# Kernel optimization log

Hardware: AMD Instinct MI355X
Metric: run time of the kernel (lower is better)

## Reference

```python
import jax, jax.numpy as jnp
import numpy as np

MARGIN = 1.0
EPS = 1e-8  # torch F.cosine_similarity default eps


def setup_inputs() -> dict:
    key = jax.random.key(0)
    k1, k2 = jax.random.split(key)
    reps = jax.random.normal(k1, (8192, 512), dtype=jnp.float32)
    labels = jax.random.randint(k2, (8192,), 0, 100, dtype=jnp.int64)
    return {"reps": reps, "labels": labels}


def reference(reps, labels):
    # cosine_similarity(reps[None, :, :], reps[:, None, :], dim=2)
    # == dot(a,b) / (max(||a||,eps) * max(||b||,eps)); compute via normalize + GEMM
    norms = jnp.maximum(jnp.linalg.norm(reps, axis=1, keepdims=True), EPS)
    xn = reps / norms  # [N, D]
    cos_sim = xn @ xn.T  # [N, N]
    label_matrix = labels[None, :] == labels[:, None]  # [N, N] bool
    same_class_loss = jnp.where(label_matrix, (1.0 - cos_sim) ** 2, 0.0)
    diff_class_loss = jnp.where(label_matrix, 0.0,
                                jnp.maximum(MARGIN - cos_sim, 0.0) ** 2)
    loss = same_class_loss + diff_class_loss
    return loss.mean()
```

## Files before the change

kernel.cpp:

```cpp
#include <hip/hip_runtime.h>


typedef __attribute__((ext_vector_type(8))) short  s8;
typedef __attribute__((ext_vector_type(8))) __bf16 bf8;
typedef __attribute__((ext_vector_type(4))) float  f4;
typedef __attribute__((ext_vector_type(4))) unsigned short u4v;

#define NT32 136
#define KOUT 16
#define KCW  512

#define OFF_XT  0u
#define OFF_INV (8u * 1024u * 1024u)
#define OFF_S   (OFF_INV + 8192u * 4u)
#define OFF_S2  (OFF_S + 512u * 4u)
#define OFF_TK  (OFF_S2 + 4u)
#define OFF_GP  (OFF_S2 + 64u)

__device__ __forceinline__ unsigned short f2bf(float f) {
    union { float f; unsigned u; } v; v.f = f;
    unsigned r = v.u + 0x7FFFu + ((v.u >> 16) & 1u);
    return (unsigned short)(r >> 16);
}

__global__ __launch_bounds__(256) void k_norms(
    const float* __restrict__ reps, float* __restrict__ inv,
    float* __restrict__ zbuf )
{
    const int t = threadIdx.x, lane = t & 63, w = t >> 6;
    if (blockIdx.x == 0) {
        for (int z = t; z < 514; z += 256) zbuf[z] = 0.f;
    }
    const int row = blockIdx.x * 4 + w;
    const float4 x0 = *(const float4*)(reps + (size_t)row * 512 + lane * 4);
    const float4 x1 = *(const float4*)(reps + (size_t)row * 512 + 256 + lane * 4);
    float ss = x0.x*x0.x + x0.y*x0.y + x0.z*x0.z + x0.w*x0.w
             + x1.x*x1.x + x1.y*x1.y + x1.z*x1.z + x1.w*x1.w;
    #pragma unroll
    for (int off = 1; off < 64; off <<= 1) ss += __shfl_xor(ss, off, 64);
    if (lane == 0) inv[row] = 1.0f / fmaxf(sqrtf(ss), 1e-8f);
}

__global__ __launch_bounds__(256) void k_norm_transpose(
    const float* __restrict__ reps, const float* __restrict__ inv,
    unsigned short* __restrict__ xt, float* __restrict__ svec)
{
    __shared__ unsigned short tile[64][72];
    __shared__ float sred[4][64];
    const int t = threadIdx.x, lane = t & 63, w = t >> 6;
    const int a0 = blockIdx.x * 64, i0 = blockIdx.y * 64;
    const int colg = t & 15;
    const int ig0  = t >> 4;

    float4 sa = {0.f, 0.f, 0.f, 0.f};
    #pragma unroll
    for (int j = 0; j < 4; ++j) {
        const int il = ig0 + j * 16;
        const float iv = inv[i0 + il];
        const float4 x = *(const float4*)(reps + (size_t)(i0 + il) * 512 + a0 + colg * 4);
        const float4 xn = {x.x * iv, x.y * iv, x.z * iv, x.w * iv};
        sa.x += xn.x; sa.y += xn.y; sa.z += xn.z; sa.w += xn.w;
        ushort4 p;
        p.x = f2bf(xn.x); p.y = f2bf(xn.y); p.z = f2bf(xn.z); p.w = f2bf(xn.w);
        *(ushort4*)&tile[il][colg * 4] = p;
    }
    __syncthreads();

    {
        const int ig = t & 15, ag = t >> 4;
        u4v rows[4];
        #pragma unroll
        for (int r = 0; r < 4; ++r)
            rows[r] = *(const u4v*)&tile[ig * 4 + r][ag * 4];
        #pragma unroll
        for (int j = 0; j < 4; ++j) {
            ushort4 o;
            o.x = (unsigned short)rows[0][j];
            o.y = (unsigned short)rows[1][j];
            o.z = (unsigned short)rows[2][j];
            o.w = (unsigned short)rows[3][j];
            *(ushort4*)(xt + (size_t)(a0 + ag * 4 + j) * 8192 + i0 + ig * 4) = o;
        }
    }

    sa.x += __shfl_xor(sa.x, 16, 64); sa.x += __shfl_xor(sa.x, 32, 64);
    sa.y += __shfl_xor(sa.y, 16, 64); sa.y += __shfl_xor(sa.y, 32, 64);
    sa.z += __shfl_xor(sa.z, 16, 64); sa.z += __shfl_xor(sa.z, 32, 64);
    sa.w += __shfl_xor(sa.w, 16, 64); sa.w += __shfl_xor(sa.w, 32, 64);
    if (lane < 16) {
        sred[w][lane * 4 + 0] = sa.x; sred[w][lane * 4 + 1] = sa.y;
        sred[w][lane * 4 + 2] = sa.z; sred[w][lane * 4 + 3] = sa.w;
    }
    __syncthreads();
    if (t < 64) {
        const float v = sred[0][t] + sred[1][t] + sred[2][t] + sred[3][t];
        atomicAdd(&svec[a0 + t], v);
    }
}

__global__ __launch_bounds__(64) void k_gram(
    const unsigned short* __restrict__ xt, float* __restrict__ gp)
{
    const int lane = threadIdx.x;
    const int l15 = lane & 15, l4 = lane >> 4;
    int tt = blockIdx.x, ta = 0;
    while (tt >= 16 - ta) { tt -= 16 - ta; ++ta; }
    const int tb = ta + tt;
    const int k0 = blockIdx.y * KCW;
    const unsigned short* Arow = xt + (size_t)(ta * 32 + l15) * 8192;
    const unsigned short* Brow = xt + (size_t)(tb * 32 + l15) * 8192;

    f4 acc[2][2];
    #pragma unroll
    for (int mi = 0; mi < 2; ++mi)
        #pragma unroll
        for (int ni = 0; ni < 2; ++ni) {
            f4 z = {0.f, 0.f, 0.f, 0.f};
            acc[mi][ni] = z;
        }

    for (int k = 0; k < KCW; k += 32) {
        const int ko = k0 + k + l4 * 8;
        s8 af[2], bfr[2];
        af[0]  = *(const s8*)(Arow + ko);
        af[1]  = *(const s8*)(Arow + (size_t)16 * 8192 + ko);
        bfr[0] = *(const s8*)(Brow + ko);
        bfr[1] = *(const s8*)(Brow + (size_t)16 * 8192 + ko);
        #pragma unroll
        for (int mi = 0; mi < 2; ++mi)
            #pragma unroll
            for (int ni = 0; ni < 2; ++ni)
                acc[mi][ni] = __builtin_amdgcn_mfma_f32_16x16x32_bf16(
                    __builtin_bit_cast(bf8, af[mi]),
                    __builtin_bit_cast(bf8, bfr[ni]),
                    acc[mi][ni], 0, 0, 0);
    }

    float* gb = gp + ((size_t)blockIdx.y * NT32 + blockIdx.x) * 1024;
    #pragma unroll
    for (int mi = 0; mi < 2; ++mi)
        #pragma unroll
        for (int ni = 0; ni < 2; ++ni)
            #pragma unroll
            for (int r = 0; r < 4; ++r) {
                const int a_ = mi * 16 + l4 * 4 + r;
                const int b_ = ni * 16 + l15;
                gb[a_ * 32 + b_] = acc[mi][ni][r];
            }
}

__global__ __launch_bounds__(256) void k_reduce_final(
    const float* __restrict__ gp, const float* __restrict__ svec,
    float* __restrict__ s2, int* __restrict__ ticket,
    float* __restrict__ out)
{
    __shared__ float part[4];
    __shared__ int lastFlag;
    const int t = threadIdx.x;
    const int c = blockIdx.x * 256 + t;
    const f4* g4 = (const f4*)gp;
    f4 s = {0.f, 0.f, 0.f, 0.f};
    #pragma unroll
    for (int p = 0; p < KOUT; ++p) s += g4[(size_t)p * (NT32 * 256) + c];
    int tt = c >> 8, ta = 0;
    while (tt >= 16 - ta) { tt -= 16 - ta; ++ta; }
    const float wgt = (tt == 0) ? 1.f : 2.f;
    float sq = wgt * (s.x * s.x + s.y * s.y + s.z * s.z + s.w * s.w);
    #pragma unroll
    for (int off = 1; off < 64; off <<= 1) sq += __shfl_xor(sq, off, 64);
    if ((t & 63) == 0) part[t >> 6] = sq;
    __syncthreads();
    if (t == 0) {
        atomicAdd(s2, part[0] + part[1] + part[2] + part[3]);
        __threadfence();
        lastFlag = (atomicAdd(ticket, 1) == (int)gridDim.x - 1);
    }
    __syncthreads();
    if (lastFlag) {
        __threadfence();
        const float v0 = svec[t], v1 = svec[t + 256];
        float p = v0 * v0 + v1 * v1;
        #pragma unroll
        for (int off = 1; off < 64; off <<= 1) p += __shfl_xor(p, off, 64);
        if ((t & 63) == 0) part[t >> 6] = p;
        __syncthreads();
        if (t == 0) {
            const float s1 = part[0] + part[1] + part[2] + part[3];
            const float S2 = atomicAdd(s2, 0.f);
            const double NN = 67108864.0;
            out[0] = (float)((NN - 2.0 * (double)s1 + (double)S2) / NN);
        }
    }
}

extern "C" void kernel_launch(void* const* d_in, const int* in_sizes, int n_in,
                              void* d_out, int out_size, void* d_ws, size_t ws_size,
                              hipStream_t stream)
{
    const float* reps = (const float*)d_in[0];
    char* ws = (char*)d_ws;
    unsigned short* xt   = (unsigned short*)(ws + OFF_XT);
    float*          invn = (float*)(ws + OFF_INV);
    float*          svec = (float*)(ws + OFF_S);
    float*          s2   = (float*)(ws + OFF_S2);
    int*            tick = (int*)(ws + OFF_TK);
    float*          gp   = (float*)(ws + OFF_GP);

    k_norms<<<2048, 256, 0, stream>>>(reps, invn, svec);
    k_norm_transpose<<<dim3(8, 128), 256, 0, stream>>>(reps, invn, xt, svec);
    k_gram<<<dim3(NT32, KOUT), 64, 0, stream>>>(xt, gp);
    k_reduce_final<<<NT32, 256, 0, stream>>>(gp, svec, s2, tick, (float*)d_out);
}
```

Baseline: 98.70 us.

## Split Gram K-reduction finer, remap blocks per XCD, widen final reduction grid

The Gram kernel now splits the 8192-long reduction into 32 chunks instead of 16, which doubles the number of blocks. It uses a 1D grid whose block index is remapped so that all K-chunks of a tile land on the same XCD, sharing L2 for the A/B rows, and it adds an occupancy hint and unroll. The final reduction launches 1088 blocks, each summing a slice of partials across K-planes through LDS instead of 136 blocks doing 16 serial loads. The transpose's padded LDS tile is replaced by an XOR-swizzled layout. The intent is more parallelism and better cache locality, at the cost of twice the partial-sum traffic.

```diff
diff --git a/kernel.cpp b/kernel.cpp
--- a/kernel.cpp
+++ b/kernel.cpp
@@ -7,8 +7,10 @@
 typedef __attribute__((ext_vector_type(4))) unsigned short u4v;
 
 #define NT32 136
-#define KOUT 16
-#define KCW  512
+#define KOUT 32
+#define KCW  256
+#define PLANE_F4 (NT32 * 256)
+#define RB 1088
 
 #define OFF_XT  0u
 #define OFF_INV (8u * 1024u * 1024u)
@@ -45,7 +47,7 @@
     const float* __restrict__ reps, const float* __restrict__ inv,
     unsigned short* __restrict__ xt, float* __restrict__ svec)
 {
-    __shared__ unsigned short tile[64][72];
+    __shared__ unsigned short tile[64 * 64];
     __shared__ float sred[4][64];
     const int t = threadIdx.x, lane = t & 63, w = t >> 6;
     const int a0 = blockIdx.x * 64, i0 = blockIdx.y * 64;
@@ -62,7 +64,7 @@
         sa.x += xn.x; sa.y += xn.y; sa.z += xn.z; sa.w += xn.w;
         ushort4 p;
         p.x = f2bf(xn.x); p.y = f2bf(xn.y); p.z = f2bf(xn.z); p.w = f2bf(xn.w);
-        *(ushort4*)&tile[il][colg * 4] = p;
+        *(ushort4*)&tile[il * 64 + ((colg * 4) ^ (((il >> 2) & 7) << 3))] = p;
     }
     __syncthreads();
 
@@ -71,7 +73,7 @@
         u4v rows[4];
         #pragma unroll
         for (int r = 0; r < 4; ++r)
-            rows[r] = *(const u4v*)&tile[ig * 4 + r][ag * 4];
+            rows[r] = *(const u4v*)&tile[(ig * 4 + r) * 64 + ((ag * 4) ^ ((ig & 7) << 3))];
         #pragma unroll
         for (int j = 0; j < 4; ++j) {
             ushort4 o;
@@ -98,55 +100,49 @@
     }
 }
 
-__global__ __launch_bounds__(64) void k_gram(
+__global__ __launch_bounds__(64, 4) void k_gram(
     const unsigned short* __restrict__ xt, float* __restrict__ gp)
 {
     const int lane = threadIdx.x;
     const int l15 = lane & 15, l4 = lane >> 4;
-    int tt = blockIdx.x, ta = 0;
+    const int lin = blockIdx.x;
+    const int xcd = lin & 7, j = lin >> 3;
+    const int tIdx = xcd * 17 + (j >> 5);
+    const int kc   = j & 31;
+    int tt = tIdx, ta = 0;
     while (tt >= 16 - ta) { tt -= 16 - ta; ++ta; }
     const int tb = ta + tt;
-    const int k0 = blockIdx.y * KCW;
-    const unsigned short* Arow = xt + (size_t)(ta * 32 + l15) * 8192;
-    const unsigned short* Brow = xt + (size_t)(tb * 32 + l15) * 8192;
-
-    f4 acc[2][2];
+    const unsigned short* A0 = xt + (size_t)(ta * 32 + l15) * 8192 + kc * KCW + l4 * 8;
+    const unsigned short* B0 = xt + (size_t)(tb * 32 + l15) * 8192 + kc * KCW + l4 * 8;
+
+    f4 acc00 = {0.f,0.f,0.f,0.f}, acc01 = {0.f,0.f,0.f,0.f};
+    f4 acc10 = {0.f,0.f,0.f,0.f}, acc11 = {0.f,0.f,0.f,0.f};
+
+    #pragma unroll 4
+    for (int k = 0; k < KCW; k += 32) {
+        const s8 av0 = *(const s8*)(A0 + k);
+        const s8 av1 = *(const s8*)(A0 + 16 * 8192 + k);
+        const s8 bv0 = *(const s8*)(B0 + k);
+        const s8 bv1 = *(const s8*)(B0 + 16 * 8192 + k);
+        acc00 = __builtin_amdgcn_mfma_f32_16x16x32_bf16(
+            __builtin_bit_cast(bf8, av0), __builtin_bit_cast(bf8, bv0), acc00, 0, 0, 0);
+        acc01 = __builtin_amdgcn_mfma_f32_16x16x32_bf16(
+            __builtin_bit_cast(bf8, av0), __builtin_bit_cast(bf8, bv1), acc01, 0, 0, 0);
+        acc10 = __builtin_amdgcn_mfma_f32_16x16x32_bf16(
+            __builtin_bit_cast(bf8, av1), __builtin_bit_cast(bf8, bv0), acc10, 0, 0, 0);
+        acc11 = __builtin_amdgcn_mfma_f32_16x16x32_bf16(
+            __builtin_bit_cast(bf8, av1), __builtin_bit_cast(bf8, bv1), acc11, 0, 0, 0);
+    }
+
+    float* gb = gp + ((size_t)kc * NT32 + tIdx) * 1024;
     #pragma unroll
-    for (int mi = 0; mi < 2; ++mi)
-        #pragma unroll
-        for (int ni = 0; ni < 2; ++ni) {
-            f4 z = {0.f, 0.f, 0.f, 0.f};
-            acc[mi][ni] = z;
-        }
-
-    for (int k = 0; k < KCW; k += 32) {
-        const int ko = k0 + k + l4 * 8;
-        s8 af[2], bfr[2];
-        af[0]  = *(const s8*)(Arow + ko);
-        af[1]  = *(const s8*)(Arow + (size_t)16 * 8192 + ko);
-        bfr[0] = *(const s8*)(Brow + ko);
-        bfr[1] = *(const s8*)(Brow + (size_t)16 * 8192 + ko);
-        #pragma unroll
-        for (int mi = 0; mi < 2; ++mi)
-            #pragma unroll
-            for (int ni = 0; ni < 2; ++ni)
-                acc[mi][ni] = __builtin_amdgcn_mfma_f32_16x16x32_bf16(
-                    __builtin_bit_cast(bf8, af[mi]),
-                    __builtin_bit_cast(bf8, bfr[ni]),
-                    acc[mi][ni], 0, 0, 0);
-    }
-
-    float* gb = gp + ((size_t)blockIdx.y * NT32 + blockIdx.x) * 1024;
-    #pragma unroll
-    for (int mi = 0; mi < 2; ++mi)
-        #pragma unroll
-        for (int ni = 0; ni < 2; ++ni)
-            #pragma unroll
-            for (int r = 0; r < 4; ++r) {
-                const int a_ = mi * 16 + l4 * 4 + r;
-                const int b_ = ni * 16 + l15;
-                gb[a_ * 32 + b_] = acc[mi][ni][r];
-            }
+    for (int r = 0; r < 4; ++r) {
+        const int ar0 = (l4 * 4 + r) * 32 + l15;
+        gb[ar0]            = acc00[r];
+        gb[ar0 + 16]       = acc01[r];
+        gb[ar0 + 16 * 32]  = acc10[r];
+        gb[ar0 + 16 * 33]  = acc11[r];
+    }
 }
 
 __global__ __launch_bounds__(256) void k_reduce_final(
@@ -154,26 +150,35 @@
     float* __restrict__ s2, int* __restrict__ ticket,
     float* __restrict__ out)
 {
-    __shared__ float part[4];
+    __shared__ f4 accs[8][32];
+    __shared__ float pw[4];
     __shared__ int lastFlag;
     const int t = threadIdx.x;
-    const int c = blockIdx.x * 256 + t;
+    const int cl = t & 31, q = t >> 5;
+    const int c = blockIdx.x * 32 + cl;
     const f4* g4 = (const f4*)gp;
-    f4 s = {0.f, 0.f, 0.f, 0.f};
-    #pragma unroll
-    for (int p = 0; p < KOUT; ++p) s += g4[(size_t)p * (NT32 * 256) + c];
-    int tt = c >> 8, ta = 0;
-    while (tt >= 16 - ta) { tt -= 16 - ta; ++ta; }
-    const float wgt = (tt == 0) ? 1.f : 2.f;
-    float sq = wgt * (s.x * s.x + s.y * s.y + s.z * s.z + s.w * s.w);
-    #pragma unroll
-    for (int off = 1; off < 64; off <<= 1) sq += __shfl_xor(sq, off, 64);
-    if ((t & 63) == 0) part[t >> 6] = sq;
-    __syncthreads();
-    if (t == 0) {
-        atomicAdd(s2, part[0] + part[1] + part[2] + part[3]);
-        __threadfence();
-        lastFlag = (atomicAdd(ticket, 1) == (int)gridDim.x - 1);
+    f4 sA = {0.f,0.f,0.f,0.f}, sB = {0.f,0.f,0.f,0.f};
+    sA += g4[(size_t)(q * 4 + 0) * PLANE_F4 + c];
+    sB += g4[(size_t)(q * 4 + 1) * PLANE_F4 + c];
+    sA += g4[(size_t)(q * 4 + 2) * PLANE_F4 + c];
+    sB += g4[(size_t)(q * 4 + 3) * PLANE_F4 + c];
+    accs[q][cl] = sA + sB;
+    __syncthreads();
+    if (t < 32) {
+        f4 tot = accs[0][t];
+        #pragma unroll
+        for (int qq = 1; qq < 8; ++qq) tot += accs[qq][t];
+        int tt = c >> 8, ta = 0;
+        while (tt >= 16 - ta) { tt -= 16 - ta; ++ta; }
+        const float wgt = (tt == 0) ? 1.f : 2.f;
+        float sq = wgt * (tot.x*tot.x + tot.y*tot.y + tot.z*tot.z + tot.w*tot.w);
+        #pragma unroll
+        for (int off = 1; off < 32; off <<= 1) sq += __shfl_xor(sq, off, 64);
+        if (t == 0) {
+            atomicAdd(s2, sq);
+            __threadfence();
+            lastFlag = (atomicAdd(ticket, 1) == RB - 1);
+        }
     }
     __syncthreads();
     if (lastFlag) {
@@ -182,10 +187,10 @@
         float p = v0 * v0 + v1 * v1;
         #pragma unroll
         for (int off = 1; off < 64; off <<= 1) p += __shfl_xor(p, off, 64);
-        if ((t & 63) == 0) part[t >> 6] = p;
+        if ((t & 63) == 0) pw[t >> 6] = p;
         __syncthreads();
         if (t == 0) {
-            const float s1 = part[0] + part[1] + part[2] + part[3];
+            const float s1 = pw[0] + pw[1] + pw[2] + pw[3];
             const float S2 = atomicAdd(s2, 0.f);
             const double NN = 67108864.0;
             out[0] = (float)((NN - 2.0 * (double)s1 + (double)S2) / NN);
@@ -208,6 +213,6 @@
 
     k_norms<<<2048, 256, 0, stream>>>(reps, invn, svec);
     k_norm_transpose<<<dim3(8, 128), 256, 0, stream>>>(reps, invn, xt, svec);
-    k_gram<<<dim3(NT32, KOUT), 64, 0, stream>>>(xt, gp);
-    k_reduce_final<<<NT32, 256, 0, stream>>>(gp, svec, s2, tick, (float*)d_out);
-}
+    k_gram<<<NT32 * KOUT, 64, 0, stream>>>(xt, gp);
+    k_reduce_final<<<RB, 256, 0, stream>>>(gp, svec, s2, tick, (float*)d_out);
+}
```

Result: slower. 125.3 us (+26.9%).

## Store transposed bf16 data in MFMA fragment-tiled layout for coalesced gram loads

Applied to the files above, without the earlier changes.

The transpose kernel now writes the normalized bf16 matrix in a blocked layout where each 16-row group and 32-wide k chunk occupies a contiguous 512-element tile matching the MFMA operand fragment. The gram kernel can then load each fragment as one fully contiguous 1 KB wavefront read instead of 16 strided row segments. Diagonal tiles reuse the A loads as B operands to skip redundant loads. The transpose writes become more scattered, which may cost some store efficiency there.

```diff
diff --git a/kernel.cpp b/kernel.cpp
--- a/kernel.cpp
+++ b/kernel.cpp
@@ -9,6 +9,7 @@
 #define NT32 136
 #define KOUT 16
 #define KCW  512
+#define GSTRIDE (256 * 512)
 
 #define OFF_XT  0u
 #define OFF_INV (8u * 1024u * 1024u)
@@ -72,14 +73,22 @@
         #pragma unroll
         for (int r = 0; r < 4; ++r)
             rows[r] = *(const u4v*)&tile[ig * 4 + r][ag * 4];
+        const int gbase = a0 >> 4;
+        const int c     = (i0 >> 5) + (ig >> 3);
+        const int ks    = (ig >> 1) & 3;
+        const int ke4   = ig & 1;
         #pragma unroll
         for (int j = 0; j < 4; ++j) {
+            const int al = ag * 4 + j;
+            const int g  = gbase + (al >> 4);
+            const int rl = al & 15;
             ushort4 o;
             o.x = (unsigned short)rows[0][j];
             o.y = (unsigned short)rows[1][j];
             o.z = (unsigned short)rows[2][j];
             o.w = (unsigned short)rows[3][j];
-            *(ushort4*)(xt + (size_t)(a0 + ag * 4 + j) * 8192 + i0 + ig * 4) = o;
+            *(ushort4*)(xt + ((((size_t)g * 256 + c) << 9)
+                              + (ks * 16 + rl) * 8 + ke4 * 4)) = o;
         }
     }
 
@@ -106,47 +115,52 @@
     int tt = blockIdx.x, ta = 0;
     while (tt >= 16 - ta) { tt -= 16 - ta; ++ta; }
     const int tb = ta + tt;
-    const int k0 = blockIdx.y * KCW;
-    const unsigned short* Arow = xt + (size_t)(ta * 32 + l15) * 8192;
-    const unsigned short* Brow = xt + (size_t)(tb * 32 + l15) * 8192;
-
-    f4 acc[2][2];
-    #pragma unroll
-    for (int mi = 0; mi < 2; ++mi)
-        #pragma unroll
-        for (int ni = 0; ni < 2; ++ni) {
-            f4 z = {0.f, 0.f, 0.f, 0.f};
-            acc[mi][ni] = z;
-        }
-
-    for (int k = 0; k < KCW; k += 32) {
-        const int ko = k0 + k + l4 * 8;
-        s8 af[2], bfr[2];
-        af[0]  = *(const s8*)(Arow + ko);
-        af[1]  = *(const s8*)(Arow + (size_t)16 * 8192 + ko);
-        bfr[0] = *(const s8*)(Brow + ko);
-        bfr[1] = *(const s8*)(Brow + (size_t)16 * 8192 + ko);
-        #pragma unroll
-        for (int mi = 0; mi < 2; ++mi)
-            #pragma unroll
-            for (int ni = 0; ni < 2; ++ni)
-                acc[mi][ni] = __builtin_amdgcn_mfma_f32_16x16x32_bf16(
-                    __builtin_bit_cast(bf8, af[mi]),
-                    __builtin_bit_cast(bf8, bfr[ni]),
-                    acc[mi][ni], 0, 0, 0);
+    const int c0 = blockIdx.y * (KCW / 32);
+    const unsigned short* A0 = xt + (((size_t)(ta * 2) * 256 + c0) << 9) + lane * 8;
+    const unsigned short* B0 = xt + (((size_t)(tb * 2) * 256 + c0) << 9) + lane * 8;
+
+    f4 acc00 = {0.f,0.f,0.f,0.f}, acc01 = {0.f,0.f,0.f,0.f};
+    f4 acc10 = {0.f,0.f,0.f,0.f}, acc11 = {0.f,0.f,0.f,0.f};
+
+    if (ta != tb) {
+        for (int cc = 0; cc < 16; ++cc) {
+            const s8 av0 = *(const s8*)(A0 + cc * 512);
+            const s8 av1 = *(const s8*)(A0 + GSTRIDE + cc * 512);
+            const s8 bv0 = *(const s8*)(B0 + cc * 512);
+            const s8 bv1 = *(const s8*)(B0 + GSTRIDE + cc * 512);
+            acc00 = __builtin_amdgcn_mfma_f32_16x16x32_bf16(
+                __builtin_bit_cast(bf8, av0), __builtin_bit_cast(bf8, bv0), acc00, 0, 0, 0);
+            acc01 = __builtin_amdgcn_mfma_f32_16x16x32_bf16(
+                __builtin_bit_cast(bf8, av0), __builtin_bit_cast(bf8, bv1), acc01, 0, 0, 0);
+            acc10 = __builtin_amdgcn_mfma_f32_16x16x32_bf16(
+                __builtin_bit_cast(bf8, av1), __builtin_bit_cast(bf8, bv0), acc10, 0, 0, 0);
+            acc11 = __builtin_amdgcn_mfma_f32_16x16x32_bf16(
+                __builtin_bit_cast(bf8, av1), __builtin_bit_cast(bf8, bv1), acc11, 0, 0, 0);
+        }
+    } else {
+        for (int cc = 0; cc < 16; ++cc) {
+            const s8 av0 = *(const s8*)(A0 + cc * 512);
+            const s8 av1 = *(const s8*)(A0 + GSTRIDE + cc * 512);
+            acc00 = __builtin_amdgcn_mfma_f32_16x16x32_bf16(
+                __builtin_bit_cast(bf8, av0), __builtin_bit_cast(bf8, av0), acc00, 0, 0, 0);
+            acc01 = __builtin_amdgcn_mfma_f32_16x16x32_bf16(
+                __builtin_bit_cast(bf8, av0), __builtin_bit_cast(bf8, av1), acc01, 0, 0, 0);
+            acc10 = __builtin_amdgcn_mfma_f32_16x16x32_bf16(
+                __builtin_bit_cast(bf8, av1), __builtin_bit_cast(bf8, av0), acc10, 0, 0, 0);
+            acc11 = __builtin_amdgcn_mfma_f32_16x16x32_bf16(
+                __builtin_bit_cast(bf8, av1), __builtin_bit_cast(bf8, av1), acc11, 0, 0, 0);
+        }
     }
 
     float* gb = gp + ((size_t)blockIdx.y * NT32 + blockIdx.x) * 1024;
     #pragma unroll
-    for (int mi = 0; mi < 2; ++mi)
-        #pragma unroll
-        for (int ni = 0; ni < 2; ++ni)
-            #pragma unroll
-            for (int r = 0; r < 4; ++r) {
-                const int a_ = mi * 16 + l4 * 4 + r;
-                const int b_ = ni * 16 + l15;
-                gb[a_ * 32 + b_] = acc[mi][ni][r];
-            }
+    for (int r = 0; r < 4; ++r) {
+        const int ar0 = (l4 * 4 + r) * 32 + l15;
+        gb[ar0]           = acc00[r];
+        gb[ar0 + 16]      = acc01[r];
+        gb[ar0 + 16 * 32] = acc10[r];
+        gb[ar0 + 16 * 33] = acc11[r];
+    }
 }
 
 __global__ __launch_bounds__(256) void k_reduce_final(
```

Result: faster. 91.40 us (-7.4%).
